# Performance work log

Hardware: AMD Instinct MI355X
Metric: run time of the kernel (lower is better)

Reference implementation:

```python
import jax, jax.numpy as jnp
import numpy as np

TOTAL_OUTPUTS = 50000
PER_CLASS = 224
N_CLASSES = int(np.ceil(TOTAL_OUTPUTS / PER_CLASS))  # 224
B, T, D = 4, 512, 1024


def setup_inputs() -> dict:
    key = jax.random.key(0)
    k1, k2, k3, k4 = jax.random.split(key, 4)
    scale_top = float(np.sqrt(2.0 / (D + N_CLASSES)))      # glorot-ish
    scale_bot = float(np.sqrt(2.0 / (D + PER_CLASS)))
    return {
        "x": jax.random.normal(k1, (B, T, D), dtype=jnp.float32),
        "target": jax.random.randint(k2, (B, T), 0, TOTAL_OUTPUTS, dtype=jnp.int32),
        "top_weights": jax.random.normal(k3, (D, N_CLASSES), dtype=jnp.float32) * scale_top,
        "top_bias": jnp.zeros((N_CLASSES,), dtype=jnp.float32),
        "bottom_weights": jax.random.normal(k4, (N_CLASSES, D, PER_CLASS), dtype=jnp.float32) * scale_bot,
        "bottom_bias": jnp.zeros((N_CLASSES, PER_CLASS), dtype=jnp.float32),
    }


def reference(x, target, top_weights, top_bias, bottom_weights, bottom_bias):
    # Flatten (batch, time) -> samples, as in call()
    b, t, d = x.shape
    xf = x.reshape(b * t, d)                      # (N, D)
    tf = target.reshape(-1)                       # (N,)

    # Top-level dense softmax over classes
    p_top = jax.nn.softmax(xf @ top_weights + top_bias, axis=-1)  # (N, n_classes)

    # Decompose target into (class, within-class) indices, as in theano h_softmax
    cls = tf // PER_CLASS                         # (N,)
    within = tf % PER_CLASS                       # (N,)

    # Gather per-sample bottom expert weights and compute small GEMM + softmax
    w_c = bottom_weights[cls]                     # (N, D, per_class)  <- irregular gather
    b_c = bottom_bias[cls]                        # (N, per_class)
    bot_logits = jnp.einsum('nd,ndp->np', xf, w_c) + b_c
    p_bot = jax.nn.softmax(bot_logits, axis=-1)   # (N, per_class)

    n_idx = jnp.arange(xf.shape[0])
    px = p_top[n_idx, cls] * p_bot[n_idx, within]  # (N,) target probabilities
    return px.reshape(b, t, -1)                    # (B, T, 1)
```

## Files before the change

### kernel.cpp

```cpp
#include <hip/hip_runtime.h>

#define NSAMP 2048
#define DIM 1024
#define NCLS 224
#define PERCLS 224
#define CH 16
#define KSL 128
#define NSLICE 4
#define TOPBLKS ((NSAMP / CH) * NSLICE)
#define BOTBLKS (NCLS * NSLICE)

struct Ws {
  int cls[NSAMP];
  int within[NSAMP];
  int order[NSAMP];
  int offsets[NCLS + 1];
  int pad_[3];
  float top_part[NSLICE][NSAMP][NCLS];
  float bot_part[NSLICE][NSAMP][PERCLS];
};

__global__ __launch_bounds__(256) void prep_kernel(const int* __restrict__ target,
                                                   Ws* __restrict__ ws) {
  __shared__ int cnt[NCLS];
  __shared__ int cur[NCLS];
  __shared__ int sc[256];
  int tid = threadIdx.x;
  for (int c = tid; c < NCLS; c += 256) cnt[c] = 0;
  __syncthreads();
  for (int n = tid; n < NSAMP; n += 256) {
    int t = target[n];
    int c = t / PERCLS;
    ws->cls[n] = c;
    ws->within[n] = t - c * PERCLS;
    atomicAdd(&cnt[c], 1);
  }
  __syncthreads();
  int v = (tid < NCLS) ? cnt[tid] : 0;
  sc[tid] = v;
  __syncthreads();
  for (int off = 1; off < 256; off <<= 1) {
    int a = (tid >= off) ? sc[tid - off] : 0;
    __syncthreads();
    sc[tid] += a;
    __syncthreads();
  }
  if (tid < NCLS) {
    int excl = sc[tid] - cnt[tid];
    ws->offsets[tid] = excl;
    cur[tid] = excl;
  }
  if (tid == 0) ws->offsets[NCLS] = NSAMP;
  __syncthreads();
  for (int n = tid; n < NSAMP; n += 256) {
    int c = ws->cls[n];
    int pos = atomicAdd(&cur[c], 1);
    ws->order[pos] = n;
  }
}

__global__ __launch_bounds__(256) void partial_kernel(const float* __restrict__ x,
                                                      const float* __restrict__ tw,
                                                      const float* __restrict__ bw,
                                                      Ws* __restrict__ ws) {
  __shared__ float xs[2][CH][KSL];
  const int tid = threadIdx.x;
  const int lane = tid & 63;
  const int wave = tid >> 6;
  const int kg = wave >> 1;
  const int sg = wave & 1;
  const int bid = blockIdx.x;

  const bool is_top = bid < TOPBLKS;
  int n0 = 0, c = 0, bs, start = 0, K = CH;
  if (is_top) {
    bs = bid & 3;
    n0 = (bid >> 2) * CH;
  } else {
    int b = bid - TOPBLKS;
    bs = b & 3;
    c = b >> 2;
    start = ws->offsets[c];
    K = ws->offsets[c + 1] - start;
    if (K == 0) return;
  }
  const int kbase = bs * (2 * KSL) + kg * KSL;
  const float* Wbase = is_top ? (tw + (size_t)kbase * NCLS)
                              : (bw + (size_t)c * (DIM * PERCLS) + (size_t)kbase * PERCLS);
  const float4* W4 = (const float4*)Wbase + lane;
  const float4* xb = (const float4*)xs + kg * 512 + sg * 256;
  float4* red4 = (float4*)xs;

#define FMA4(A, XQ, W0, W1, W2, W3)                                   \
  A.x = fmaf(XQ.x, W0.x, A.x); A.y = fmaf(XQ.x, W0.y, A.y);           \
  A.z = fmaf(XQ.x, W0.z, A.z); A.w = fmaf(XQ.x, W0.w, A.w);           \
  A.x = fmaf(XQ.y, W1.x, A.x); A.y = fmaf(XQ.y, W1.y, A.y);           \
  A.z = fmaf(XQ.y, W1.z, A.z); A.w = fmaf(XQ.y, W1.w, A.w);           \
  A.x = fmaf(XQ.z, W2.x, A.x); A.y = fmaf(XQ.z, W2.y, A.y);           \
  A.z = fmaf(XQ.z, W2.z, A.z); A.w = fmaf(XQ.z, W2.w, A.w);           \
  A.x = fmaf(XQ.w, W3.x, A.x); A.y = fmaf(XQ.w, W3.y, A.y);           \
  A.z = fmaf(XQ.w, W3.z, A.z); A.w = fmaf(XQ.w, W3.w, A.w)

#define COMPUTE(W0, W1, W2, W3, G)                                    \
  { _Pragma("unroll")                                                 \
    for (int s = 0; s < 8; ++s) {                                     \
      float4 xq = xb[s * 32 + (G)];                                   \
      FMA4(acc[s], xq, W0, W1, W2, W3);                               \
    } }

  for (int chunk = 0; chunk < K; chunk += CH) {
    const int S = min(CH, K - chunk);
    __syncthreads();

#pragma unroll
    for (int pass = 0; pass < 4; ++pass) {
      int i = tid + pass * 256;
      int kgx = i >> 9;
      int ss = (i >> 5) & 15;
      int q = i & 31;
      int n;
      if (is_top) n = n0 + ss;
      else        n = ws->order[start + min(chunk + ss, K - 1)];
      ((float4*)xs)[i] =
          *(const float4*)(x + (size_t)n * DIM + bs * (2 * KSL) + kgx * KSL + q * 4);
    }
    __syncthreads();

    float4 acc[8];
#pragma unroll
    for (int s = 0; s < 8; ++s) acc[s] = make_float4(0.f, 0.f, 0.f, 0.f);

    if (lane < 56) {
      const float4* Wp = W4;
      float4 wa0, wa1, wa2, wa3, wb0, wb1, wb2, wb3;
      wa0 = Wp[0]; wa1 = Wp[56]; wa2 = Wp[112]; wa3 = Wp[168]; Wp += 224;
#pragma unroll 5
      for (int gp = 0; gp < 15; ++gp) {
        wb0 = Wp[0]; wb1 = Wp[56]; wb2 = Wp[112]; wb3 = Wp[168]; Wp += 224;
        COMPUTE(wa0, wa1, wa2, wa3, 2 * gp);
        wa0 = Wp[0]; wa1 = Wp[56]; wa2 = Wp[112]; wa3 = Wp[168]; Wp += 224;
        COMPUTE(wb0, wb1, wb2, wb3, 2 * gp + 1);
      }
      wb0 = Wp[0]; wb1 = Wp[56]; wb2 = Wp[112]; wb3 = Wp[168];
      COMPUTE(wa0, wa1, wa2, wa3, 30);
      COMPUTE(wb0, wb1, wb2, wb3, 31);
    }

    __syncthreads();
    if (kg == 1 && lane < 56) {
#pragma unroll
      for (int s = 0; s < 8; ++s) red4[(sg * 8 + s) * 56 + lane] = acc[s];
    }
    __syncthreads();
    if (kg == 0 && lane < 56) {
      if (is_top) {
#pragma unroll
        for (int s = 0; s < 8; ++s) {
          float4 o = red4[(sg * 8 + s) * 56 + lane];
          acc[s].x += o.x; acc[s].y += o.y; acc[s].z += o.z; acc[s].w += o.w;
          *(float4*)&ws->top_part[bs][n0 + sg * 8 + s][lane * 4] = acc[s];
        }
      } else {
#pragma unroll
        for (int s = 0; s < 8; ++s) {
          int sl = sg * 8 + s;
          if (sl < S) {
            float4 o = red4[sl * 56 + lane];
            acc[s].x += o.x; acc[s].y += o.y; acc[s].z += o.z; acc[s].w += o.w;
            int n = ws->order[start + chunk + sl];
            *(float4*)&ws->bot_part[bs][n][lane * 4] = acc[s];
          }
        }
      }
    }
  }
#undef COMPUTE
#undef FMA4
}

__global__ __launch_bounds__(256) void final_kernel(const float* __restrict__ tb,
                                                    const float* __restrict__ bb,
                                                    const Ws* __restrict__ ws,
                                                    float* __restrict__ out) {
  __shared__ float lt[8][NCLS];
  __shared__ float lb[8][NCLS];
  const int tid = threadIdx.x;
  const int n0 = blockIdx.x * 8;
  const int p = tid;

  if (p < NCLS) {
    float tbias = tb[p];
#pragma unroll
    for (int s = 0; s < 8; ++s) {
      int n = n0 + s;
      int c = ws->cls[n];
      float t = tbias;
      float b = bb[(size_t)c * PERCLS + p];
#pragma unroll
      for (int dc = 0; dc < NSLICE; ++dc) t += ws->top_part[dc][n][p];
#pragma unroll
      for (int dc = 0; dc < NSLICE; ++dc) b += ws->bot_part[dc][n][p];
      lt[s][p] = t;
      lb[s][p] = b;
    }
  }
  __syncthreads();

  const int wv = tid >> 6, lane = tid & 63;
  for (int s = wv * 2; s < wv * 2 + 2; ++s) {
    const int n = n0 + s;
    float v[4], mx = -INFINITY;
#pragma unroll
    for (int j = 0; j < 4; ++j) {
      int pp = lane + 64 * j;
      v[j] = (pp < NCLS) ? lt[s][pp] : -INFINITY;
      mx = fmaxf(mx, v[j]);
    }
#pragma unroll
    for (int m = 32; m >= 1; m >>= 1) mx = fmaxf(mx, __shfl_xor(mx, m));
    float sum = 0.f;
#pragma unroll
    for (int j = 0; j < 4; ++j) {
      int pp = lane + 64 * j;
      if (pp < NCLS) sum += expf(v[j] - mx);
    }
#pragma unroll
    for (int m = 32; m >= 1; m >>= 1) sum += __shfl_xor(sum, m);
    float pt = expf(lt[s][ws->cls[n]] - mx) / sum;

    float mb = -INFINITY;
#pragma unroll
    for (int j = 0; j < 4; ++j) {
      int pp = lane + 64 * j;
      v[j] = (pp < NCLS) ? lb[s][pp] : -INFINITY;
      mb = fmaxf(mb, v[j]);
    }
#pragma unroll
    for (int m = 32; m >= 1; m >>= 1) mb = fmaxf(mb, __shfl_xor(mb, m));
    float sb = 0.f;
#pragma unroll
    for (int j = 0; j < 4; ++j) {
      int pp = lane + 64 * j;
      if (pp < NCLS) sb += expf(v[j] - mb);
    }
#pragma unroll
    for (int m = 32; m >= 1; m >>= 1) sb += __shfl_xor(sb, m);
    float pb = expf(lb[s][ws->within[n]] - mb) / sb;

    if (lane == 0) out[n] = pt * pb;
  }
}

extern "C" void kernel_launch(void* const* d_in, const int* in_sizes, int n_in,
                              void* d_out, int out_size, void* d_ws, size_t ws_size,
                              hipStream_t stream) {
  const float* x  = (const float*)d_in[0];
  const int* tgt  = (const int*)d_in[1];
  const float* tw = (const float*)d_in[2];
  const float* tb = (const float*)d_in[3];
  const float* bw = (const float*)d_in[4];
  const float* bb = (const float*)d_in[5];
  float* out = (float*)d_out;
  Ws* ws = (Ws*)d_ws;

  prep_kernel<<<1, 256, 0, stream>>>(tgt, ws);
  partial_kernel<<<TOPBLKS + BOTBLKS, 256, 0, stream>>>(x, tw, bw, ws);
  final_kernel<<<NSAMP / 8, 256, 0, stream>>>(tb, bb, ws, out);
}
```

Baseline: 88.80 us.

## Stage weight tiles into LDS via async global_load_lds with a triple-buffered pipeline

Result: slower. 131.3 us (+47.9%).

```diff
diff --git a/kernel.cpp b/kernel.cpp
--- a/kernel.cpp
+++ b/kernel.cpp
@@ -5,10 +5,11 @@
 #define NCLS 224
 #define PERCLS 224
 #define CH 16
-#define KSL 128
+#define KSL 256
 #define NSLICE 4
 #define TOPBLKS ((NSAMP / CH) * NSLICE)
 #define BOTBLKS (NCLS * NSLICE)
+#define NTILE 32
 
 struct Ws {
   int cls[NSAMP];
@@ -63,12 +64,13 @@
                                                       const float* __restrict__ tw,
                                                       const float* __restrict__ bw,
                                                       Ws* __restrict__ ws) {
-  __shared__ float xs[2][CH][KSL];
+  __shared__ float xs[CH][KSL];
+  __shared__ float w_lds[4 * 2048];
   const int tid = threadIdx.x;
   const int lane = tid & 63;
   const int wave = tid >> 6;
-  const int kg = wave >> 1;
-  const int sg = wave & 1;
+  const int sg = wave >> 1;
+  const int ch = wave & 1;
   const int bid = blockIdx.x;
 
   const bool is_top = bid < TOPBLKS;
@@ -84,29 +86,23 @@
     K = ws->offsets[c + 1] - start;
     if (K == 0) return;
   }
-  const int kbase = bs * (2 * KSL) + kg * KSL;
-  const float* Wbase = is_top ? (tw + (size_t)kbase * NCLS)
-                              : (bw + (size_t)c * (DIM * PERCLS) + (size_t)kbase * PERCLS);
-  const float4* W4 = (const float4*)Wbase + lane;
-  const float4* xb = (const float4*)xs + kg * 512 + sg * 256;
-  float4* red4 = (float4*)xs;
-
-#define FMA4(A, XQ, W0, W1, W2, W3)                                   \
-  A.x = fmaf(XQ.x, W0.x, A.x); A.y = fmaf(XQ.x, W0.y, A.y);           \
-  A.z = fmaf(XQ.x, W0.z, A.z); A.w = fmaf(XQ.x, W0.w, A.w);           \
-  A.x = fmaf(XQ.y, W1.x, A.x); A.y = fmaf(XQ.y, W1.y, A.y);           \
-  A.z = fmaf(XQ.y, W1.z, A.z); A.w = fmaf(XQ.y, W1.w, A.w);           \
-  A.x = fmaf(XQ.z, W2.x, A.x); A.y = fmaf(XQ.z, W2.y, A.y);           \
-  A.z = fmaf(XQ.z, W2.z, A.z); A.w = fmaf(XQ.z, W2.w, A.w);           \
-  A.x = fmaf(XQ.w, W3.x, A.x); A.y = fmaf(XQ.w, W3.y, A.y);           \
-  A.z = fmaf(XQ.w, W3.z, A.z); A.w = fmaf(XQ.w, W3.w, A.w)
-
-#define COMPUTE(W0, W1, W2, W3, G)                                    \
-  { _Pragma("unroll")                                                 \
-    for (int s = 0; s < 8; ++s) {                                     \
-      float4 xq = xb[s * 32 + (G)];                                   \
-      FMA4(acc[s], xq, W0, W1, W2, W3);                               \
-    } }
+  const float* Wslice = is_top ? (tw + (size_t)(bs * KSL) * NCLS)
+                               : (bw + (size_t)c * (DIM * PERCLS) + (size_t)(bs * KSL) * PERCLS);
+  const int u0 = 2 * wave;
+  const int u1s = (2 * wave + 1 < 7) ? (2 * wave + 1) : 6;
+  const int u1d = 2 * wave + 1;
+
+  typedef const __attribute__((address_space(1))) unsigned int gu32;
+  typedef __attribute__((address_space(3))) unsigned int lu32;
+
+  auto stage_tile = [&](int t) {
+    const float* s0 = Wslice + (size_t)t * 1792 + u0 * 256 + lane * 4;
+    const float* s1 = Wslice + (size_t)t * 1792 + u1s * 256 + lane * 4;
+    float* d0 = &w_lds[(t & 3) * 2048 + u0 * 256];
+    float* d1 = &w_lds[(t & 3) * 2048 + u1d * 256];
+    __builtin_amdgcn_global_load_lds((gu32*)s0, (lu32*)d0, 16, 0, 0);
+    __builtin_amdgcn_global_load_lds((gu32*)s1, (lu32*)d1, 16, 0, 0);
+  };
 
   for (int chunk = 0; chunk < K; chunk += CH) {
     const int S = min(CH, K - chunk);
@@ -115,67 +111,83 @@
 #pragma unroll
     for (int pass = 0; pass < 4; ++pass) {
       int i = tid + pass * 256;
-      int kgx = i >> 9;
-      int ss = (i >> 5) & 15;
-      int q = i & 31;
+      int ss = i >> 6;
+      int q = i & 63;
       int n;
       if (is_top) n = n0 + ss;
       else        n = ws->order[start + min(chunk + ss, K - 1)];
-      ((float4*)xs)[i] =
-          *(const float4*)(x + (size_t)n * DIM + bs * (2 * KSL) + kgx * KSL + q * 4);
-    }
-    __syncthreads();
-
-    float4 acc[8];
-#pragma unroll
-    for (int s = 0; s < 8; ++s) acc[s] = make_float4(0.f, 0.f, 0.f, 0.f);
+      ((float4*)xs)[i] = *(const float4*)(x + (size_t)n * DIM + bs * KSL + q * 4);
+    }
+    __syncthreads();
+
+    float2 acc[8];
+#pragma unroll
+    for (int s = 0; s < 8; ++s) acc[s] = make_float2(0.f, 0.f);
+
+    const int co = ch * 112 + lane * 2;
+
+    auto compute_tile = [&](int t) {
+      if (lane < 56) {
+        const float* wb = &w_lds[(t & 3) * 2048];
+#pragma unroll
+        for (int g = 0; g < 2; ++g) {
+          float2 w0 = *(const float2*)&wb[(g * 4 + 0) * 224 + co];
+          float2 w1 = *(const float2*)&wb[(g * 4 + 1) * 224 + co];
+          float2 w2 = *(const float2*)&wb[(g * 4 + 2) * 224 + co];
+          float2 w3 = *(const float2*)&wb[(g * 4 + 3) * 224 + co];
+#pragma unroll
+          for (int s = 0; s < 8; ++s) {
+            float4 xv = *(const float4*)&xs[sg * 8 + s][t * 8 + g * 4];
+            acc[s].x = fmaf(xv.x, w0.x, acc[s].x); acc[s].y = fmaf(xv.x, w0.y, acc[s].y);
+            acc[s].x = fmaf(xv.y, w1.x, acc[s].x); acc[s].y = fmaf(xv.y, w1.y, acc[s].y);
+            acc[s].x = fmaf(xv.z, w2.x, acc[s].x); acc[s].y = fmaf(xv.z, w2.y, acc[s].y);
+            acc[s].x = fmaf(xv.w, w3.x, acc[s].x); acc[s].y = fmaf(xv.w, w3.y, acc[s].y);
+          }
+        }
+      }
+    };
+
+    stage_tile(0);
+    stage_tile(1);
+    stage_tile(2);
+
+    for (int t = 0; t < NTILE - 3; ++t) {
+      asm volatile("s_waitcnt vmcnt(4)" ::: "memory");
+      __builtin_amdgcn_sched_barrier(0);
+      __builtin_amdgcn_s_barrier();
+      stage_tile(t + 3);
+      compute_tile(t);
+    }
+    asm volatile("s_waitcnt vmcnt(4)" ::: "memory");
+    __builtin_amdgcn_sched_barrier(0);
+    __builtin_amdgcn_s_barrier();
+    compute_tile(NTILE - 3);
+    asm volatile("s_waitcnt vmcnt(2)" ::: "memory");
+    __builtin_amdgcn_sched_barrier(0);
+    __builtin_amdgcn_s_barrier();
+    compute_tile(NTILE - 2);
+    asm volatile("s_waitcnt vmcnt(0)" ::: "memory");
+    __builtin_amdgcn_sched_barrier(0);
+    __builtin_amdgcn_s_barrier();
+    compute_tile(NTILE - 1);
 
     if (lane < 56) {
-      const float4* Wp = W4;
-      float4 wa0, wa1, wa2, wa3, wb0, wb1, wb2, wb3;
-      wa0 = Wp[0]; wa1 = Wp[56]; wa2 = Wp[112]; wa3 = Wp[168]; Wp += 224;
-#pragma unroll 5
-      for (int gp = 0; gp < 15; ++gp) {
-        wb0 = Wp[0]; wb1 = Wp[56]; wb2 = Wp[112]; wb3 = Wp[168]; Wp += 224;
-        COMPUTE(wa0, wa1, wa2, wa3, 2 * gp);
-        wa0 = Wp[0]; wa1 = Wp[56]; wa2 = Wp[112]; wa3 = Wp[168]; Wp += 224;
-        COMPUTE(wb0, wb1, wb2, wb3, 2 * gp + 1);
-      }
-      wb0 = Wp[0]; wb1 = Wp[56]; wb2 = Wp[112]; wb3 = Wp[168];
-      COMPUTE(wa0, wa1, wa2, wa3, 30);
-      COMPUTE(wb0, wb1, wb2, wb3, 31);
-    }
-
-    __syncthreads();
-    if (kg == 1 && lane < 56) {
-#pragma unroll
-      for (int s = 0; s < 8; ++s) red4[(sg * 8 + s) * 56 + lane] = acc[s];
-    }
-    __syncthreads();
-    if (kg == 0 && lane < 56) {
       if (is_top) {
 #pragma unroll
-        for (int s = 0; s < 8; ++s) {
-          float4 o = red4[(sg * 8 + s) * 56 + lane];
-          acc[s].x += o.x; acc[s].y += o.y; acc[s].z += o.z; acc[s].w += o.w;
-          *(float4*)&ws->top_part[bs][n0 + sg * 8 + s][lane * 4] = acc[s];
-        }
+        for (int s = 0; s < 8; ++s)
+          *(float2*)&ws->top_part[bs][n0 + sg * 8 + s][co] = acc[s];
       } else {
 #pragma unroll
         for (int s = 0; s < 8; ++s) {
           int sl = sg * 8 + s;
           if (sl < S) {
-            float4 o = red4[sl * 56 + lane];
-            acc[s].x += o.x; acc[s].y += o.y; acc[s].z += o.z; acc[s].w += o.w;
             int n = ws->order[start + chunk + sl];
-            *(float4*)&ws->bot_part[bs][n][lane * 4] = acc[s];
+            *(float2*)&ws->bot_part[bs][n][co] = acc[s];
           }
         }
       }
     }
   }
-#undef COMPUTE
-#undef FMA4
 }
 
 __global__ __launch_bounds__(256) void final_kernel(const float* __restrict__ tb,
```
